# Optimization experiments

Hardware: AMD Instinct MI355X
Metric: run time of the kernel (lower is better)

The kernel has to match this reference:

```python
import jax, jax.numpy as jnp
import numpy as np

N_NODES = 100000
N_EDGES = 1600000
D_IN = 128
D_HID = 128
D_OUT = 32


def setup_inputs() -> dict:
    key = jax.random.key(0)
    ks = jax.random.split(key, 10)
    x = jax.random.normal(ks[0], (N_NODES, D_IN), dtype=jnp.float32)
    edge_index = jax.random.randint(ks[1], (2, N_EDGES), 0, N_NODES, dtype=jnp.int64)
    s = 0.05
    return {
        "x": x,
        "edge_index": edge_index,
        "Wl0": jax.random.normal(ks[2], (D_IN, D_HID), jnp.float32) * s,
        "bl0": jnp.zeros((D_HID,), jnp.float32),
        "Wr0": jax.random.normal(ks[3], (D_IN, D_HID), jnp.float32) * s,
        "Wl1": jax.random.normal(ks[4], (D_HID, D_HID), jnp.float32) * s,
        "bl1": jnp.zeros((D_HID,), jnp.float32),
        "Wr1": jax.random.normal(ks[5], (D_HID, D_HID), jnp.float32) * s,
        "Wl2": jax.random.normal(ks[6], (D_HID, D_OUT), jnp.float32) * s,
        "bl2": jnp.zeros((D_OUT,), jnp.float32),
        "Wr2": jax.random.normal(ks[7], (D_HID, D_OUT), jnp.float32) * s,
    }


def _sage_conv(x, src, dst, Wl, bl, Wr):
    # PyG SAGEConv (aggr='mean', root_weight=True):
    # out[i] = lin_l(mean_{j in N(i)} x_j) + lin_r(x_i)
    n = x.shape[0]
    msgs = x[src]                                        # [E, F] gather
    agg = jax.ops.segment_sum(msgs, dst, num_segments=n) # [N, F] scatter-add
    deg = jax.ops.segment_sum(jnp.ones((src.shape[0],), x.dtype), dst, num_segments=n)
    mean = agg / jnp.maximum(deg, 1.0)[:, None]
    return mean @ Wl + bl + x @ Wr


def reference(x, edge_index, Wl0, bl0, Wr0, Wl1, bl1, Wr1, Wl2, bl2, Wr2):
    src, dst = edge_index[0], edge_index[1]
    h = jax.nn.relu(_sage_conv(x, src, dst, Wl0, bl0, Wr0))
    h = jax.nn.relu(_sage_conv(h, src, dst, Wl1, bl1, Wr1))
    h = _sage_conv(h, src, dst, Wl2, bl2, Wr2)
    return jax.nn.log_softmax(h, axis=1)
```

## Files before the change

### kernel.cpp

```cpp
#include <hip/hip_runtime.h>
#include <hip/hip_bf16.h>
#include <math.h>

#define NN 100000
#define NE 1600000

#define NCB 391
#define EB  8192
#define SCT 512
#define HBK 64
#define NSB 196
#define WPB 144

typedef __attribute__((ext_vector_type(8))) short short8;
typedef __attribute__((ext_vector_type(4))) float f32x4;

__device__ __forceinline__ unsigned short f2bf(float f) {
  union { float f; unsigned int i; } v; v.f = f;
  unsigned int i = v.i;
  unsigned int r = (i + 0x7FFFu + ((i >> 16) & 1u)) >> 16;
  return (unsigned short)r;
}
__device__ __forceinline__ float bflo(unsigned int u) {
  union { unsigned int i; float f; } v; v.i = u << 16; return v.f;
}
__device__ __forceinline__ float bfhi(unsigned int u) {
  union { unsigned int i; float f; } v; v.i = u & 0xFFFF0000u; return v.f;
}
__device__ __forceinline__ float bf1(unsigned short u) {
  union { unsigned int i; float f; } v; v.i = ((unsigned int)u) << 16; return v.f;
}

__global__ __launch_bounds__(512) void k_prep(
    const int* __restrict__ dst, int* __restrict__ part,
    const float* __restrict__ Wl0, const float* __restrict__ Wr0,
    const float* __restrict__ Wl1, const float* __restrict__ Wr1,
    const float* __restrict__ Wl2, const float* __restrict__ Wr2,
    unsigned short* __restrict__ B0, unsigned short* __restrict__ B1,
    unsigned short* __restrict__ B2) {
  if (blockIdx.x < HBK) {
    __shared__ int h[NCB];
    for (int i = threadIdx.x; i < NCB; i += 512) h[i] = 0;
    __syncthreads();
    int stride = HBK * 512;
    for (int e = blockIdx.x * 512 + threadIdx.x; e < NE; e += stride) {
      int d = dst[e];
      d = d < 0 ? 0 : (d >= NN ? NN - 1 : d);
      atomicAdd(&h[d >> 8], 1);
    }
    __syncthreads();
    for (int i = threadIdx.x; i < NCB; i += 512) part[blockIdx.x * NCB + i] = h[i];
  } else {
    int idx = (blockIdx.x - HBK) * 512 + threadIdx.x;
    if (idx < 32768) {
      int n = idx >> 7, k = idx & 127;
      float v = (n < 128) ? Wl0[k * 128 + n] : Wr0[k * 128 + (n - 128)];
      B0[idx] = f2bf(v);
    } else if (idx < 65536) {
      int j = idx - 32768;
      int n = j >> 7, k = j & 127;
      float v = (n < 128) ? Wl1[k * 128 + n] : Wr1[k * 128 + (n - 128)];
      B1[j] = f2bf(v);
    } else if (idx < 73728) {
      int j = idx - 65536;
      int n = j >> 7, k = j & 127;
      float v = (n < 32) ? Wl2[k * 32 + n] : Wr2[k * 32 + (n - 32)];
      B2[j] = f2bf(v);
    }
  }
}

__global__ __launch_bounds__(512) void k_cscan(const int* __restrict__ part,
                                               int* __restrict__ cboff,
                                               int* __restrict__ ccur,
                                               int* __restrict__ csroff) {
  __shared__ int sd[512];
  int t = threadIdx.x;
  int v = 0;
  if (t < NCB) {
    int s0 = 0, s1 = 0, s2 = 0, s3 = 0;
    #pragma unroll 4
    for (int k = 0; k < HBK; k += 4) {
      s0 += part[(k + 0) * NCB + t];
      s1 += part[(k + 1) * NCB + t];
      s2 += part[(k + 2) * NCB + t];
      s3 += part[(k + 3) * NCB + t];
    }
    v = (s0 + s1) + (s2 + s3);
    ccur[t] = 0;
  }
  sd[t] = v;
  __syncthreads();
  for (int st = 1; st < 512; st <<= 1) {
    int x = (t >= st) ? sd[t - st] : 0;
    __syncthreads();
    sd[t] += x;
    __syncthreads();
  }
  if (t < NCB) cboff[t] = sd[t] - v;
  if (t == NCB - 1) { cboff[NCB] = sd[t]; csroff[NN] = sd[t]; }
}


__device__ __forceinline__ void cscatter_body(
    char* smem, int bid,
    const int* __restrict__ src, const int* __restrict__ dst,
    const int* __restrict__ cboff, int* __restrict__ ccur,
    unsigned int* __restrict__ ebuf) {
  int* lh = (int*)smem;
  unsigned int* sRank = (unsigned int*)(smem + 1600);
  unsigned int* sPay  = (unsigned int*)(smem + 1600 + EB * 4);
  int t = threadIdx.x;
  int base = bid * EB;
  for (int i = t; i < NCB; i += SCT) lh[i] = 0;
  __syncthreads();
  #pragma unroll
  for (int i = 0; i < EB / SCT; i++) {
    int idx = i * SCT + t;
    int e = base + idx;
    unsigned int rk = 0xFFFFFFFFu, pv = 0;
    if (e < NE) {
      int d = dst[e];
      d = d < 0 ? 0 : (d >= NN ? NN - 1 : d);
      int s = src[e];
      s = s < 0 ? 0 : (s >= NN ? NN - 1 : s);
      int cb = d >> 8;
      int r = atomicAdd(&lh[cb], 1);
      rk = (((unsigned int)cb) << 13) | (unsigned int)r;
      pv = (((unsigned int)(d & 255)) << 17) | (unsigned int)s;
    }
    sRank[idx] = rk;
    sPay[idx]  = pv;
  }
  __syncthreads();
  for (int i = t; i < NCB; i += SCT) {
    int c = lh[i];
    int g = c ? atomicAdd(&ccur[i], c) : 0;
    lh[i] = cboff[i] + g;
  }
  __syncthreads();
  #pragma unroll
  for (int i = 0; i < EB / SCT; i++) {
    int idx = i * SCT + t;
    unsigned int rk = sRank[idx];
    if (rk != 0xFFFFFFFFu) {
      int cb = rk >> 13;
      int r  = rk & 0x1FFF;
      ebuf[lh[cb] + r] = sPay[idx];
    }
  }
}

__device__ __forceinline__ void mgemm0_body(
    char* smem, int bid, const float* __restrict__ A,
    const unsigned short* __restrict__ Bp, const float* __restrict__ bias,
    unsigned short* __restrict__ yl, unsigned short* __restrict__ yr) {
  unsigned short* sA = (unsigned short*)smem;
  int tid = threadIdx.x;
  int nb  = bid * 128;

  #pragma unroll
  for (int i = 0; i < 8; i++) {
    int j = i * 512 + tid;
    int m = j >> 5;
    int k4 = (j & 31) * 4;
    int gn = nb + m;
    float4 v = make_float4(0.f, 0.f, 0.f, 0.f);
    if (gn < NN) v = *(const float4*)&A[gn * 128 + k4];
    unsigned int p0 = (unsigned int)f2bf(v.x) | ((unsigned int)f2bf(v.y) << 16);
    unsigned int p1 = (unsigned int)f2bf(v.z) | ((unsigned int)f2bf(v.w) << 16);
    *(uint2*)&sA[m * 136 + k4] = make_uint2(p0, p1);
  }
  __syncthreads();

  int wave = tid >> 6, lane = tid & 63;
  int l15 = lane & 15, lq = lane >> 4;
  int wm = wave & 1, wn = wave >> 1;
  int mbase = wm * 64;
  int nbase = wn * 64;

  f32x4 acc[4][4];
  #pragma unroll
  for (int mi = 0; mi < 4; mi++)
    #pragma unroll
    for (int ni = 0; ni < 4; ni++) acc[mi][ni] = (f32x4){0.f, 0.f, 0.f, 0.f};

  #pragma unroll
  for (int kc = 0; kc < 4; kc++) {
    int k0 = kc * 32 + lq * 8;
    short8 af[4], bfr[4];
    #pragma unroll
    for (int ni = 0; ni < 4; ni++)
      bfr[ni] = *(const short8*)&Bp[(nbase + ni * 16 + l15) * 128 + k0];
    #pragma unroll
    for (int mi = 0; mi < 4; mi++)
      af[mi] = *(const short8*)&sA[(mbase + mi * 16 + l15) * 136 + k0];
    #pragma unroll
    for (int mi = 0; mi < 4; mi++)
      #pragma unroll
      for (int ni = 0; ni < 4; ni++)
        acc[mi][ni] = __builtin_amdgcn_mfma_f32_16x16x32_bf16(
            af[mi], bfr[ni], acc[mi][ni], 0, 0, 0);
  }

  #pragma unroll
  for (int mi = 0; mi < 4; mi++) {
    #pragma unroll
    for (int ni = 0; ni < 4; ni++) {
      int n = nbase + ni * 16 + l15;
      #pragma unroll
      for (int r = 0; r < 4; r++) {
        int gn = nb + mbase + mi * 16 + lq * 4 + r;
        if (gn < NN) {
          float v = acc[mi][ni][r];
          if (n < 128) {
            yl[(size_t)gn * 128 + n] = f2bf(v);
          } else {
            int n2 = n - 128;
            yr[(size_t)gn * 128 + n2] = f2bf(v + bias[n2]);
          }
        }
      }
    }
  }
}

__global__ __launch_bounds__(512) void k_scatgemm(
    const int* __restrict__ src, const int* __restrict__ dst,
    const int* __restrict__ cboff, int* __restrict__ ccur,
    unsigned int* __restrict__ ebuf,
    const float* __restrict__ x, const unsigned short* __restrict__ B0,
    const float* __restrict__ bias,
    unsigned short* __restrict__ yl, unsigned short* __restrict__ yr) {
  __shared__ char smem[1600 + EB * 8];
  if (blockIdx.x < NSB) {
    cscatter_body(smem, blockIdx.x, src, dst, cboff, ccur, ebuf);
  } else {
    mgemm0_body(smem, blockIdx.x - NSB, x, B0, bias, yl, yr);
  }
}

__global__ __launch_bounds__(256) void k_crefine(
    const unsigned int* __restrict__ ebuf, const int* __restrict__ cboff,
    int* __restrict__ csroff, float* __restrict__ invd,
    int* __restrict__ csrsrc) {
  __shared__ int lh[256], pos[256], cur[256];
  int b = blockIdx.x, t = threadIdx.x;
  lh[t] = 0; cur[t] = 0;
  __syncthreads();
  int beg = cboff[b], end = cboff[b + 1];
  for (int i = beg + t; i < end; i += 256) atomicAdd(&lh[ebuf[i] >> 17], 1);
  __syncthreads();
  int v = lh[t];
  pos[t] = v;
  __syncthreads();
  for (int st = 1; st < 256; st <<= 1) {
    int x = (t >= st) ? pos[t - st] : 0;
    __syncthreads();
    pos[t] += x;
    __syncthreads();
  }
  int nid = b * 256 + t;
  int mybase = cboff[b] + pos[t] - v;
  if (nid < NN) {
    csroff[nid] = mybase;
    invd[nid] = 1.0f / (float)(v < 1 ? 1 : v);
  }
  __syncthreads();
  pos[t] = mybase;
  __syncthreads();
  for (int i = beg + t; i < end; i += 256) {
    unsigned int u = ebuf[i];
    int local = u >> 17;
    int r = atomicAdd(&cur[local], 1);
    csrsrc[pos[local] + r] = (int)(u & 0x1FFFFu);
  }
}

template <int NC>
__global__ __launch_bounds__(512) void k_mgemm(
    const unsigned short* __restrict__ A, const unsigned short* __restrict__ Bp,
    const float* __restrict__ bias,
    unsigned short* __restrict__ yl, unsigned short* __restrict__ yr) {
  __shared__ unsigned short sA[128 * 136];
  int tid = threadIdx.x;
  int nb  = blockIdx.x * 128;

  #pragma unroll
  for (int i = 0; i < 4; i++) {
    int j = i * 512 + tid;
    int m = j >> 4;
    int k8 = (j & 15) * 8;
    int gn = nb + m;
    uint4 v = make_uint4(0, 0, 0, 0);
    if (gn < NN) v = *(const uint4*)&A[gn * 128 + k8];
    *(uint4*)&sA[m * 136 + k8] = v;
  }
  __syncthreads();

  int wave = tid >> 6, lane = tid & 63;
  int l15 = lane & 15, lq = lane >> 4;
  constexpr int MT = (NC == 256) ? 4 : 2;
  constexpr int NT = (NC == 256) ? 4 : 2;
  int wm, wn;
  if (NC == 256) { wm = wave & 1; wn = wave >> 1; }
  else           { wm = wave >> 1; wn = wave & 1; }
  int mbase = wm * (MT * 16);
  int nbase = wn * (NT * 16);

  f32x4 acc[MT][NT];
  #pragma unroll
  for (int mi = 0; mi < MT; mi++)
    #pragma unroll
    for (int ni = 0; ni < NT; ni++) acc[mi][ni] = (f32x4){0.f, 0.f, 0.f, 0.f};

  #pragma unroll
  for (int kc = 0; kc < 4; kc++) {
    int k0 = kc * 32 + lq * 8;
    short8 af[MT], bfr[NT];
    #pragma unroll
    for (int ni = 0; ni < NT; ni++)
      bfr[ni] = *(const short8*)&Bp[(nbase + ni * 16 + l15) * 128 + k0];
    #pragma unroll
    for (int mi = 0; mi < MT; mi++)
      af[mi] = *(const short8*)&sA[(mbase + mi * 16 + l15) * 136 + k0];
    #pragma unroll
    for (int mi = 0; mi < MT; mi++)
      #pragma unroll
      for (int ni = 0; ni < NT; ni++)
        acc[mi][ni] = __builtin_amdgcn_mfma_f32_16x16x32_bf16(
            af[mi], bfr[ni], acc[mi][ni], 0, 0, 0);
  }

  constexpr int HC = NC / 2;
  #pragma unroll
  for (int mi = 0; mi < MT; mi++) {
    #pragma unroll
    for (int ni = 0; ni < NT; ni++) {
      int n = nbase + ni * 16 + l15;
      #pragma unroll
      for (int r = 0; r < 4; r++) {
        int gn = nb + mbase + mi * 16 + lq * 4 + r;
        if (gn < NN) {
          float v = acc[mi][ni][r];
          if (n < HC) {
            yl[(size_t)gn * HC + n] = f2bf(v);
          } else {
            int n2 = n - HC;
            yr[(size_t)gn * HC + n2] = f2bf(v + bias[n2]);
          }
        }
      }
    }
  }
}

__global__ __launch_bounds__(256) void k_agg128(
    const unsigned short* __restrict__ yl, const unsigned short* __restrict__ yr,
    const int* __restrict__ off, const int* __restrict__ csr,
    const float* __restrict__ invd, unsigned short* __restrict__ out, int relu) {
  int wid  = (blockIdx.x * 256 + threadIdx.x) >> 6;
  int lane = threadIdx.x & 63;
  if (wid >= NN) return;
  int beg = off[wid], end = off[wid + 1];
  const unsigned int* ylp = (const unsigned int*)yl;
  float ax0 = 0.f, ay0 = 0.f, ax1 = 0.f, ay1 = 0.f;
  float ax2 = 0.f, ay2 = 0.f, ax3 = 0.f, ay3 = 0.f;
  int e = beg;
  for (; e + 7 < end; e += 8) {
    int s0 = csr[e],     s1 = csr[e + 1], s2 = csr[e + 2], s3 = csr[e + 3];
    int s4 = csr[e + 4], s5 = csr[e + 5], s6 = csr[e + 6], s7 = csr[e + 7];
    unsigned int u0 = ylp[s0 * 64 + lane];
    unsigned int u1 = ylp[s1 * 64 + lane];
    unsigned int u2 = ylp[s2 * 64 + lane];
    unsigned int u3 = ylp[s3 * 64 + lane];
    unsigned int u4 = ylp[s4 * 64 + lane];
    unsigned int u5 = ylp[s5 * 64 + lane];
    unsigned int u6 = ylp[s6 * 64 + lane];
    unsigned int u7 = ylp[s7 * 64 + lane];
    ax0 += bflo(u0); ay0 += bfhi(u0);
    ax1 += bflo(u1); ay1 += bfhi(u1);
    ax2 += bflo(u2); ay2 += bfhi(u2);
    ax3 += bflo(u3); ay3 += bfhi(u3);
    ax0 += bflo(u4); ay0 += bfhi(u4);
    ax1 += bflo(u5); ay1 += bfhi(u5);
    ax2 += bflo(u6); ay2 += bfhi(u6);
    ax3 += bflo(u7); ay3 += bfhi(u7);
  }
  for (; e < end; e++) {
    int s = csr[e];
    unsigned int u = ylp[s * 64 + lane];
    ax0 += bflo(u); ay0 += bfhi(u);
  }
  float sc = invd[wid];
  unsigned int rv = ((const unsigned int*)yr)[wid * 64 + lane];
  float vx = ((ax0 + ax1) + (ax2 + ax3)) * sc + bflo(rv);
  float vy = ((ay0 + ay1) + (ay2 + ay3)) * sc + bfhi(rv);
  if (relu) { vx = fmaxf(vx, 0.f); vy = fmaxf(vy, 0.f); }
  ((unsigned int*)out)[wid * 64 + lane] =
      (unsigned int)f2bf(vx) | ((unsigned int)f2bf(vy) << 16);
}

__global__ __launch_bounds__(256) void k_agg32_lsm(
    const unsigned short* __restrict__ yl, const unsigned short* __restrict__ yr,
    const int* __restrict__ off, const int* __restrict__ csr,
    const float* __restrict__ invd, float* __restrict__ out) {
  int row  = (blockIdx.x * 256 + threadIdx.x) >> 5;
  int lane = threadIdx.x & 31;
  if (row >= NN) return;
  int beg = off[row], end = off[row + 1];
  float a0 = 0.f, a1 = 0.f, a2 = 0.f, a3 = 0.f;
  int e = beg;
  for (; e + 3 < end; e += 4) {
    int s0 = csr[e], s1 = csr[e + 1], s2 = csr[e + 2], s3 = csr[e + 3];
    a0 += bf1(yl[s0 * 32 + lane]);
    a1 += bf1(yl[s1 * 32 + lane]);
    a2 += bf1(yl[s2 * 32 + lane]);
    a3 += bf1(yl[s3 * 32 + lane]);
  }
  for (; e < end; e++) a0 += bf1(yl[csr[e] * 32 + lane]);
  float v = ((a0 + a1) + (a2 + a3)) * invd[row] + bf1(yr[row * 32 + lane]);
  float m = v;
  #pragma unroll
  for (int o = 16; o; o >>= 1) m = fmaxf(m, __shfl_xor(m, o, 32));
  float ex = expf(v - m);
  float s = ex;
  #pragma unroll
  for (int o = 16; o; o >>= 1) s += __shfl_xor(s, o, 32);
  out[row * 32 + lane] = v - m - logf(s);
}


extern "C" void kernel_launch(void* const* d_in, const int* in_sizes, int n_in,
                              void* d_out, int out_size, void* d_ws, size_t ws_size,
                              hipStream_t stream) {
  (void)in_sizes; (void)n_in; (void)out_size; (void)ws_size;
  const float* x   = (const float*)d_in[0];
  const int*   ei  = (const int*)d_in[1];
  const float* Wl0 = (const float*)d_in[2];
  const float* bl0 = (const float*)d_in[3];
  const float* Wr0 = (const float*)d_in[4];
  const float* Wl1 = (const float*)d_in[5];
  const float* bl1 = (const float*)d_in[6];
  const float* Wr1 = (const float*)d_in[7];
  const float* Wl2 = (const float*)d_in[8];
  const float* bl2 = (const float*)d_in[9];
  const float* Wr2 = (const float*)d_in[10];
  const int* srcI = ei;
  const int* dstI = ei + NE;

  char* w = (char*)d_ws;
  int*   ccur   = (int*)(w + (16 << 10));
  int*   cboff  = (int*)(w + (32 << 10));
  unsigned short* B0 = (unsigned short*)(w + (64 << 10));
  unsigned short* B1 = (unsigned short*)(w + (160 << 10));
  unsigned short* B2 = (unsigned short*)(w + (256 << 10));
  int*   part   = (int*)(w + (288 << 10));
  int*   csroff = (int*)(w + (512 << 10));
  float* invd   = (float*)(w + (1024 << 10));
  unsigned int* ebuf = (unsigned int*)(w + (size_t)(2) * 1024 * 1024);
  int*   csrsrc = (int*)(w + (size_t)(9) * 1024 * 1024);
  unsigned short* ylb = (unsigned short*)(w + (size_t)(16) * 1024 * 1024);
  unsigned short* yrb = (unsigned short*)(w + (size_t)(48) * 1024 * 1024);
  unsigned short* hb  = (unsigned short*)(w + (size_t)(80) * 1024 * 1024);

  dim3 gg((NN + 127) / 128);

  k_prep<<<HBK + WPB, 512, 0, stream>>>(dstI, part, Wl0, Wr0, Wl1, Wr1, Wl2, Wr2,
                                        B0, B1, B2);
  k_cscan<<<1, 512, 0, stream>>>(part, cboff, ccur, csroff);
  k_scatgemm<<<NSB + 782, 512, 0, stream>>>(srcI, dstI, cboff, ccur, ebuf,
                                            x, B0, bl0, ylb, yrb);
  k_crefine<<<NCB, 256, 0, stream>>>(ebuf, cboff, csroff, invd, csrsrc);
  k_agg128<<<(NN * 64) / 256, 256, 0, stream>>>(ylb, yrb, csroff, csrsrc, invd, hb, 1);
  k_mgemm<256><<<gg, 512, 0, stream>>>(hb, B1, bl1, ylb, yrb);
  k_agg128<<<(NN * 64) / 256, 256, 0, stream>>>(ylb, yrb, csroff, csrsrc, invd, hb, 1);
  k_mgemm<64><<<gg, 512, 0, stream>>>(hb, B2, bl2, ylb, yrb);
  k_agg32_lsm<<<(NN * 32) / 256, 256, 0, stream>>>(ylb, yrb, csroff, csrsrc, invd,
                                                   (float*)d_out);
}
```

Baseline: 450.7 us.

## Vectorize neighbor gathers with uint4/uint2 loads and per-wave CSR index broadcast

Both aggregation kernels are rewritten so each wave loads up to 64 CSR neighbor indices cooperatively and broadcasts them with shuffles. Lanes are split into groups that each gather a whole row with 16-byte (128-wide) or 8-byte (32-wide) loads, so several edges are in flight per instruction. Partial sums are combined across groups with xor-shuffles at the end. The 32-wide kernel now uses one 64-lane wave per row instead of 32 lanes. This is meant to cut per-edge index-load and small-load overhead, at the cost of extra shuffle reductions and idle lanes on low-degree rows.

```diff
diff --git a/kernel.cpp b/kernel.cpp
--- a/kernel.cpp
+++ b/kernel.cpp
@@ -355,6 +355,12 @@
   }
 }
 
+#define ACC8(u) do { \
+  a0 += bflo((u).x); a1 += bfhi((u).x); \
+  a2 += bflo((u).y); a3 += bfhi((u).y); \
+  a4 += bflo((u).z); a5 += bfhi((u).z); \
+  a6 += bflo((u).w); a7 += bfhi((u).w); } while (0)
+
 __global__ __launch_bounds__(256) void k_agg128(
     const unsigned short* __restrict__ yl, const unsigned short* __restrict__ yr,
     const int* __restrict__ off, const int* __restrict__ csr,
@@ -363,71 +369,148 @@
   int lane = threadIdx.x & 63;
   if (wid >= NN) return;
   int beg = off[wid], end = off[wid + 1];
-  const unsigned int* ylp = (const unsigned int*)yl;
-  float ax0 = 0.f, ay0 = 0.f, ax1 = 0.f, ay1 = 0.f;
-  float ax2 = 0.f, ay2 = 0.f, ax3 = 0.f, ay3 = 0.f;
-  int e = beg;
-  for (; e + 7 < end; e += 8) {
-    int s0 = csr[e],     s1 = csr[e + 1], s2 = csr[e + 2], s3 = csr[e + 3];
-    int s4 = csr[e + 4], s5 = csr[e + 5], s6 = csr[e + 6], s7 = csr[e + 7];
-    unsigned int u0 = ylp[s0 * 64 + lane];
-    unsigned int u1 = ylp[s1 * 64 + lane];
-    unsigned int u2 = ylp[s2 * 64 + lane];
-    unsigned int u3 = ylp[s3 * 64 + lane];
-    unsigned int u4 = ylp[s4 * 64 + lane];
-    unsigned int u5 = ylp[s5 * 64 + lane];
-    unsigned int u6 = ylp[s6 * 64 + lane];
-    unsigned int u7 = ylp[s7 * 64 + lane];
-    ax0 += bflo(u0); ay0 += bfhi(u0);
-    ax1 += bflo(u1); ay1 += bfhi(u1);
-    ax2 += bflo(u2); ay2 += bfhi(u2);
-    ax3 += bflo(u3); ay3 += bfhi(u3);
-    ax0 += bflo(u4); ay0 += bfhi(u4);
-    ax1 += bflo(u5); ay1 += bfhi(u5);
-    ax2 += bflo(u6); ay2 += bfhi(u6);
-    ax3 += bflo(u7); ay3 += bfhi(u7);
-  }
-  for (; e < end; e++) {
-    int s = csr[e];
-    unsigned int u = ylp[s * 64 + lane];
-    ax0 += bflo(u); ay0 += bfhi(u);
-  }
+  int deg = end - beg;
+  int q   = lane >> 4;
+  int l16 = lane & 15;
+  const uint4* ylp = (const uint4*)yl;
+
   float sc = invd[wid];
-  unsigned int rv = ((const unsigned int*)yr)[wid * 64 + lane];
-  float vx = ((ax0 + ax1) + (ax2 + ax3)) * sc + bflo(rv);
-  float vy = ((ay0 + ay1) + (ay2 + ay3)) * sc + bfhi(rv);
-  if (relu) { vx = fmaxf(vx, 0.f); vy = fmaxf(vy, 0.f); }
-  ((unsigned int*)out)[wid * 64 + lane] =
-      (unsigned int)f2bf(vx) | ((unsigned int)f2bf(vy) << 16);
-}
+  uint4 rv = ((const uint4*)yr)[wid * 16 + l16];
+
+  float a0 = 0.f, a1 = 0.f, a2 = 0.f, a3 = 0.f;
+  float a4 = 0.f, a5 = 0.f, a6 = 0.f, a7 = 0.f;
+
+  for (int w0 = 0; w0 < deg; w0 += 64) {
+    int ei = w0 + lane;
+    int sv = (ei < deg) ? csr[beg + ei] : 0;
+    int wcnt = deg - w0; if (wcnt > 64) wcnt = 64;
+    int full = wcnt >> 2;
+    int p = 0;
+    for (; p + 4 <= full; p += 4) {
+      int b = p * 4 + q;
+      int s0 = __shfl(sv, b,      64);
+      int s1 = __shfl(sv, b + 4,  64);
+      int s2 = __shfl(sv, b + 8,  64);
+      int s3 = __shfl(sv, b + 12, 64);
+      uint4 u0 = ylp[s0 * 16 + l16];
+      uint4 u1 = ylp[s1 * 16 + l16];
+      uint4 u2 = ylp[s2 * 16 + l16];
+      uint4 u3 = ylp[s3 * 16 + l16];
+      ACC8(u0); ACC8(u1); ACC8(u2); ACC8(u3);
+    }
+    for (; p < full; p++) {
+      int s0 = __shfl(sv, p * 4 + q, 64);
+      uint4 u0 = ylp[s0 * 16 + l16];
+      ACC8(u0);
+    }
+    int rem = wcnt & 3;
+    if (rem && q < rem) {
+      int s0 = __shfl(sv, full * 4 + q, 64);
+      uint4 u0 = ylp[s0 * 16 + l16];
+      ACC8(u0);
+    }
+  }
+
+  a0 += __shfl_xor(a0, 16, 64); a0 += __shfl_xor(a0, 32, 64);
+  a1 += __shfl_xor(a1, 16, 64); a1 += __shfl_xor(a1, 32, 64);
+  a2 += __shfl_xor(a2, 16, 64); a2 += __shfl_xor(a2, 32, 64);
+  a3 += __shfl_xor(a3, 16, 64); a3 += __shfl_xor(a3, 32, 64);
+  a4 += __shfl_xor(a4, 16, 64); a4 += __shfl_xor(a4, 32, 64);
+  a5 += __shfl_xor(a5, 16, 64); a5 += __shfl_xor(a5, 32, 64);
+  a6 += __shfl_xor(a6, 16, 64); a6 += __shfl_xor(a6, 32, 64);
+  a7 += __shfl_xor(a7, 16, 64); a7 += __shfl_xor(a7, 32, 64);
+
+  float v0 = a0 * sc + bflo(rv.x), v1 = a1 * sc + bfhi(rv.x);
+  float v2 = a2 * sc + bflo(rv.y), v3 = a3 * sc + bfhi(rv.y);
+  float v4 = a4 * sc + bflo(rv.z), v5 = a5 * sc + bfhi(rv.z);
+  float v6 = a6 * sc + bflo(rv.w), v7 = a7 * sc + bfhi(rv.w);
+  if (relu) {
+    v0 = fmaxf(v0, 0.f); v1 = fmaxf(v1, 0.f);
+    v2 = fmaxf(v2, 0.f); v3 = fmaxf(v3, 0.f);
+    v4 = fmaxf(v4, 0.f); v5 = fmaxf(v5, 0.f);
+    v6 = fmaxf(v6, 0.f); v7 = fmaxf(v7, 0.f);
+  }
+  if (q == 0) {
+    unsigned int p0 = (unsigned int)f2bf(v0) | ((unsigned int)f2bf(v1) << 16);
+    unsigned int p1 = (unsigned int)f2bf(v2) | ((unsigned int)f2bf(v3) << 16);
+    unsigned int p2 = (unsigned int)f2bf(v4) | ((unsigned int)f2bf(v5) << 16);
+    unsigned int p3 = (unsigned int)f2bf(v6) | ((unsigned int)f2bf(v7) << 16);
+    ((uint4*)out)[wid * 16 + l16] = make_uint4(p0, p1, p2, p3);
+  }
+}
+
+#define ACC4(u) do { \
+  a0 += bflo((u).x); a1 += bfhi((u).x); \
+  a2 += bflo((u).y); a3 += bfhi((u).y); } while (0)
 
 __global__ __launch_bounds__(256) void k_agg32_lsm(
     const unsigned short* __restrict__ yl, const unsigned short* __restrict__ yr,
     const int* __restrict__ off, const int* __restrict__ csr,
     const float* __restrict__ invd, float* __restrict__ out) {
-  int row  = (blockIdx.x * 256 + threadIdx.x) >> 5;
-  int lane = threadIdx.x & 31;
-  if (row >= NN) return;
-  int beg = off[row], end = off[row + 1];
+  int wid  = (blockIdx.x * 256 + threadIdx.x) >> 6;
+  int lane = threadIdx.x & 63;
+  if (wid >= NN) return;
+  int beg = off[wid], end = off[wid + 1];
+  int deg = end - beg;
+  int q  = lane >> 3;
+  int l8 = lane & 7;
+  const uint2* ylp = (const uint2*)yl;
+
+  float sc = invd[wid];
+  uint2 rv = ((const uint2*)yr)[wid * 8 + l8];
+
   float a0 = 0.f, a1 = 0.f, a2 = 0.f, a3 = 0.f;
-  int e = beg;
-  for (; e + 3 < end; e += 4) {
-    int s0 = csr[e], s1 = csr[e + 1], s2 = csr[e + 2], s3 = csr[e + 3];
-    a0 += bf1(yl[s0 * 32 + lane]);
-    a1 += bf1(yl[s1 * 32 + lane]);
-    a2 += bf1(yl[s2 * 32 + lane]);
-    a3 += bf1(yl[s3 * 32 + lane]);
-  }
-  for (; e < end; e++) a0 += bf1(yl[csr[e] * 32 + lane]);
-  float v = ((a0 + a1) + (a2 + a3)) * invd[row] + bf1(yr[row * 32 + lane]);
-  float m = v;
-  #pragma unroll
-  for (int o = 16; o; o >>= 1) m = fmaxf(m, __shfl_xor(m, o, 32));
-  float ex = expf(v - m);
-  float s = ex;
-  #pragma unroll
-  for (int o = 16; o; o >>= 1) s += __shfl_xor(s, o, 32);
-  out[row * 32 + lane] = v - m - logf(s);
+
+  for (int w0 = 0; w0 < deg; w0 += 64) {
+    int ei = w0 + lane;
+    int sv = (ei < deg) ? csr[beg + ei] : 0;
+    int wcnt = deg - w0; if (wcnt > 64) wcnt = 64;
+    int full = wcnt >> 3;
+    int p = 0;
+    for (; p + 2 <= full; p += 2) {
+      int b = p * 8 + q;
+      int s0 = __shfl(sv, b,     64);
+      int s1 = __shfl(sv, b + 8, 64);
+      uint2 u0 = ylp[s0 * 8 + l8];
+      uint2 u1 = ylp[s1 * 8 + l8];
+      ACC4(u0); ACC4(u1);
+    }
+    for (; p < full; p++) {
+      int s0 = __shfl(sv, p * 8 + q, 64);
+      uint2 u0 = ylp[s0 * 8 + l8];
+      ACC4(u0);
+    }
+    int rem = wcnt & 7;
+    if (rem && q < rem) {
+      int s0 = __shfl(sv, full * 8 + q, 64);
+      uint2 u0 = ylp[s0 * 8 + l8];
+      ACC4(u0);
+    }
+  }
+
+  a0 += __shfl_xor(a0, 8, 64); a0 += __shfl_xor(a0, 16, 64); a0 += __shfl_xor(a0, 32, 64);
+  a1 += __shfl_xor(a1, 8, 64); a1 += __shfl_xor(a1, 16, 64); a1 += __shfl_xor(a1, 32, 64);
+  a2 += __shfl_xor(a2, 8, 64); a2 += __shfl_xor(a2, 16, 64); a2 += __shfl_xor(a2, 32, 64);
+  a3 += __shfl_xor(a3, 8, 64); a3 += __shfl_xor(a3, 16, 64); a3 += __shfl_xor(a3, 32, 64);
+
+  float v0 = a0 * sc + bflo(rv.x), v1 = a1 * sc + bfhi(rv.x);
+  float v2 = a2 * sc + bflo(rv.y), v3 = a3 * sc + bfhi(rv.y);
+
+  float m = fmaxf(fmaxf(v0, v1), fmaxf(v2, v3));
+  m = fmaxf(m, __shfl_xor(m, 1, 64));
+  m = fmaxf(m, __shfl_xor(m, 2, 64));
+  m = fmaxf(m, __shfl_xor(m, 4, 64));
+  float e0 = expf(v0 - m), e1 = expf(v1 - m);
+  float e2 = expf(v2 - m), e3 = expf(v3 - m);
+  float s = (e0 + e1) + (e2 + e3);
+  s += __shfl_xor(s, 1, 64);
+  s += __shfl_xor(s, 2, 64);
+  s += __shfl_xor(s, 4, 64);
+  float ls = logf(s);
+  if (q == 0) {
+    float4 o = make_float4(v0 - m - ls, v1 - m - ls, v2 - m - ls, v3 - m - ls);
+    ((float4*)out)[wid * 8 + l8] = o;
+  }
 }
 
 
@@ -476,6 +559,6 @@
   k_mgemm<256><<<gg, 512, 0, stream>>>(hb, B1, bl1, ylb, yrb);
   k_agg128<<<(NN * 64) / 256, 256, 0, stream>>>(ylb, yrb, csroff, csrsrc, invd, hb, 1);
   k_mgemm<64><<<gg, 512, 0, stream>>>(hb, B2, bl2, ylb, yrb);
-  k_agg32_lsm<<<(NN * 32) / 256, 256, 0, stream>>>(ylb, yrb, csroff, csrsrc, invd,
+  k_agg32_lsm<<<(NN * 64) / 256, 256, 0, stream>>>(ylb, yrb, csroff, csrsrc, invd,
                                                    (float*)d_out);
 }
```

Measured after the change: 416.7 us. 7.5% less time.
